# Optimization experiments

Hardware: AMD Instinct MI355X
Metric: run time of the kernel (lower is better)

The kernel has to match this reference:

```python
import jax, jax.numpy as jnp
import numpy as np

B, C_IN, C_OUT, T, R, CO = 8, 64, 64, 32, 32, 32


def setup_inputs() -> dict:
    key = jax.random.key(0)
    ks = jax.random.split(key, 8)
    scale = 1.0 / np.sqrt(C_IN)  # nn.Linear default uniform(-1/sqrt(in), 1/sqrt(in))
    w = lambda k: jax.random.uniform(k, (C_OUT, C_IN), jnp.float32, -scale, scale)
    return {
        "x": jax.random.normal(ks[0], (B, C_IN, T, R, CO), jnp.float32),
        "w_self": w(ks[1]),
        "w_tp": w(ks[2]),
        "w_tm": w(ks[3]),
        "w_rp": w(ks[4]),
        "w_rm": w(ks[5]),
        "w_cp": w(ks[6]),
        "w_cm": w(ks[7]),
    }


def _proj(v, w):
    # v: [B, t, r, c, C_in], w: [C_out, C_in] (nn.Linear layout)
    return jnp.einsum('btrci,oi->btrco', v, w)


def _shift_pad(a, axis, front):
    # pad 1 slice at front (True) or back (False) along `axis` of a 5-D tensor
    pads = [(0, 0)] * 5
    pads[axis] = (1, 0) if front else (0, 1)
    return jnp.pad(a, pads)


def reference(x, w_self, w_tp, w_tm, w_rp, w_rm, w_cp, w_cm):
    xp = jnp.transpose(x, (0, 2, 3, 4, 1))  # [B, T, R, Co, C_in]
    out = _proj(xp, w_self)
    if xp.shape[1] > 1:
        out = out + _shift_pad(_proj(xp[:, :-1], w_tp), 1, True)
        out = out + _shift_pad(_proj(xp[:, 1:], w_tm), 1, False)
    if xp.shape[2] > 1:
        out = out + _shift_pad(_proj(xp[:, :, :-1], w_rp), 2, True)
        out = out + _shift_pad(_proj(xp[:, :, 1:], w_rm), 2, False)
    if xp.shape[3] > 1:
        out = out + _shift_pad(_proj(xp[:, :, :, :-1], w_cp), 3, True)
        out = out + _shift_pad(_proj(xp[:, :, :, 1:], w_cm), 3, False)
    return jnp.transpose(out, (0, 4, 1, 2, 3))  # [B, C_out, T, R, Co]
```

## Files before the change

### kernel.cpp

```cpp
#include <hip/hip_runtime.h>


#define SB 32768
#define CIN 64
#define COUT 64
#define NB 8

typedef short s16x8 __attribute__((ext_vector_type(8)));
typedef __bf16 bf16x8 __attribute__((ext_vector_type(8)));
typedef float f32x4 __attribute__((ext_vector_type(4)));

__device__ __forceinline__ unsigned f2bf(float f) {
    unsigned u = __float_as_uint(f);
    u += 0x7FFFu + ((u >> 16) & 1u);
    return u >> 16;
}
__device__ __forceinline__ unsigned pk2(float lo, float hi) {
    return f2bf(lo) | (f2bf(hi) << 16);
}

__device__ __forceinline__ void gload_lds16(const void* g, void* l) {
    __builtin_amdgcn_global_load_lds(
        (const __attribute__((address_space(1))) void*)g,
        (__attribute__((address_space(3))) void*)l, 16, 0, 0);
}

__global__ __launch_bounds__(256) void prep2_kernel(const float* __restrict__ x,
                            const float* __restrict__ w0, const float* __restrict__ w1,
                            const float* __restrict__ w2, const float* __restrict__ w3,
                            const float* __restrict__ w4, const float* __restrict__ w5,
                            const float* __restrict__ w6,
                            unsigned short* __restrict__ ws) {
    int bid = blockIdx.x;
    int tid = threadIdx.x;
    if (bid >= 4096) {
        int tap = bid - 4096;
        const float* w = (tap == 0) ? w0 : (tap == 1) ? w1 : (tap == 2) ? w2
                       : (tap == 3) ? w3 : (tap == 4) ? w4 : (tap == 5) ? w5 : w6;
        unsigned p[8];
#pragma unroll
        for (int j = 0; j < 8; ++j)
            p[j] = pk2(w[tid * 16 + 2 * j], w[tid * 16 + 2 * j + 1]);
        uint4* dp = (uint4*)(ws + tap * 4096 + tid * 16);
        dp[0] = make_uint4(p[0], p[1], p[2], p[3]);
        dp[1] = make_uint4(p[4], p[5], p[6], p[7]);
        return;
    }
    int lbid = ((bid & 7) << 9) | (bid >> 3);
    int b = lbid >> 9;
    int i = (lbid & 511) * 256 + tid;
    int cg = i & 7;
    int s = (i >> 3) * 2;
    const float* xb = x + (size_t)b * CIN * SB;
    unsigned short* xq = ws + 7 * 4096;
    unsigned pa[4], pb[4];
#pragma unroll
    for (int u = 0; u < 4; ++u) {
        int ch = cg * 8 + 2 * u;
        float2 v0 = *(const float2*)(xb + (size_t)ch * SB + s);
        float2 v1 = *(const float2*)(xb + (size_t)(ch + 1) * SB + s);
        pa[u] = pk2(v0.x, v1.x);
        pb[u] = pk2(v0.y, v1.y);
    }
    uint4* dst = (uint4*)(xq + ((size_t)b * SB + s) * 64 + cg * 8);
    dst[0] = make_uint4(pa[0], pa[1], pa[2], pa[3]);
    dst[8] = make_uint4(pb[0], pb[1], pb[2], pb[3]);
}

__global__ __launch_bounds__(256, 2) void conv9_kernel(const unsigned short* __restrict__ xq,
                                                       const unsigned short* __restrict__ wq,
                                                       float* __restrict__ out) {
    __shared__ uint4 ring[4][640];
    int bid = blockIdx.x;
    int b = bid & 7;
    int rc0 = (bid >> 3) << 4;
    int tid = threadIdx.x;
    int lane = tid & 63;
    int wv = tid >> 6;
    int lo = lane & 15;
    int quad = lane >> 4;
    const uint4* xch = (const uint4*)(xq + (size_t)b * (CIN * SB));

    bf16x8 bq[7][2];
#pragma unroll
    for (int tap = 0; tap < 7; ++tap)
#pragma unroll
        for (int ks = 0; ks < 2; ++ks) {
            const unsigned short* bp = wq + tap * 4096
                + (wv * 16 + lo) * 64 + ks * 32 + quad * 8;
            bq[tap][ks] = __builtin_bit_cast(bf16x8, *(const s16x8*)bp);
        }

    int rc = rc0 + lo;
    int rl = 32 + lo;
    int r = (rc >> 5) & 31;
    int c = rc & 31;
    bool okrm = (r > 0), okrp = (r < 31), okcm = (c > 0), okcp = (c < 31);

    auto stage = [&](int ts, int k) {
#pragma unroll
        for (int j = 0; j < 2; ++j) {
            int cid = j * 256 + tid;
            int rw = cid >> 3;
            int sc = cid & 7;
            int rcx = rc0 - 32 + rw;
            rcx = rcx < 0 ? 0 : (rcx > 1023 ? 1023 : rcx);
            const uint4* g = xch + ((size_t)(ts * 1024 + rcx) << 3) + (sc ^ (rw & 7));
            gload_lds16((const void*)g, (void*)(&ring[k][j * 256 + (wv << 6)]));
        }
        if (wv < 2) {
            int cid = 512 + tid;
            int rw = cid >> 3;
            int sc = cid & 7;
            int rcx = rc0 - 32 + rw;
            rcx = rcx > 1023 ? 1023 : rcx;
            const uint4* g = xch + ((size_t)(ts * 1024 + rcx) << 3) + (sc ^ (rw & 7));
            gload_lds16((const void*)g, (void*)(&ring[k][512 + (wv << 6)]));
        }
    };

    const s16x8 zz = {0, 0, 0, 0, 0, 0, 0, 0};
    f32x4 acc;

    auto tap_lds = [&](const uint4* slab, const bf16x8 (&bt)[2], int d, bool ok) {
#pragma unroll
        for (int ks = 0; ks < 2; ++ks) {
            int row = rl + d;
            s16x8 a = *((const s16x8*)slab + row * 8 + ((ks * 4 + quad) ^ (row & 7)));
            a = ok ? a : zz;
            bf16x8 af = __builtin_bit_cast(bf16x8, a);
            acc = __builtin_amdgcn_mfma_f32_16x16x32_bf16(af, bt[ks], acc, 0, 0, 0);
        }
    };

    stage(0, 0);
    stage(1, 1);
    __syncthreads();

    for (int t = 0; t < 32; ++t) {
        if (t + 2 < 32) stage(t + 2, (t + 2) & 3);

        acc = (f32x4){0.f, 0.f, 0.f, 0.f};
        const uint4* sc_ = &ring[t & 3][0];

        tap_lds(sc_, bq[0], 0, true);
        if (t > 0)  tap_lds(&ring[(t - 1) & 3][0], bq[1], 0, true);
        if (t < 31) tap_lds(&ring[(t + 1) & 3][0], bq[2], 0, true);
        tap_lds(sc_, bq[3], -32, okrm);
        tap_lds(sc_, bq[4], 32, okrp);
        tap_lds(sc_, bq[5], -1, okcm);
        tap_lds(sc_, bq[6], 1, okcp);

        size_t ob = ((size_t)(b * COUT + wv * 16 + lo)) * SB
                  + (size_t)t * 1024 + rc0 + quad * 4;
        *(f32x4*)(out + ob) = acc;

        __syncthreads();
    }
}

__global__ __launch_bounds__(256) void wprep_kernel(const float* __restrict__ w0,
                            const float* __restrict__ w1, const float* __restrict__ w2,
                            const float* __restrict__ w3, const float* __restrict__ w4,
                            const float* __restrict__ w5, const float* __restrict__ w6,
                            unsigned short* __restrict__ ws) {
    int tap = blockIdx.x;
    int tid = threadIdx.x;
    const float* w = (tap == 0) ? w0 : (tap == 1) ? w1 : (tap == 2) ? w2
                   : (tap == 3) ? w3 : (tap == 4) ? w4 : (tap == 5) ? w5 : w6;
    unsigned p[8];
#pragma unroll
    for (int j = 0; j < 8; ++j)
        p[j] = pk2(w[tid * 16 + 2 * j], w[tid * 16 + 2 * j + 1]);
    uint4* dp = (uint4*)(ws + tap * 4096 + tid * 16);
    dp[0] = make_uint4(p[0], p[1], p[2], p[3]);
    dp[1] = make_uint4(p[4], p[5], p[6], p[7]);
}

__global__ __launch_bounds__(256) void conv_kernel(const float* __restrict__ x,
                                                   const unsigned short* __restrict__ wq,
                                                   float* __restrict__ out) {
    __shared__ uint4 alds[2560];
    int bid = blockIdx.x;
    int b = bid >> 7;
    int sblk = (bid & 127) << 8;
    int tid = threadIdx.x;
    const float* xb = x + (size_t)b * CIN * SB;

    {
        int rl = 32 + tid;
        const float* xp = xb + sblk + tid;
#pragma unroll
        for (int c = 0; c < 4; ++c) {
            unsigned pk[8];
#pragma unroll
            for (int u = 0; u < 8; ++u)
                pk[u] = pk2(xp[(size_t)(c * 16 + 2 * u) * SB],
                            xp[(size_t)(c * 16 + 2 * u + 1) * SB]);
            alds[rl * 8 + ((2 * c) ^ (rl & 7))] = make_uint4(pk[0], pk[1], pk[2], pk[3]);
            alds[rl * 8 + ((2 * c + 1) ^ (rl & 7))] = make_uint4(pk[4], pk[5], pk[6], pk[7]);
        }
    }
    {
        int hrow = tid & 63;
        int rl = (hrow < 32) ? hrow : hrow + 256;
        int s = sblk - 32 + rl;
        s = max(0, min(SB - 1, s));
        int ic = tid >> 6;
        const float* xp = xb + s + (size_t)(ic * 16) * SB;
        unsigned pk[8];
#pragma unroll
        for (int u = 0; u < 8; ++u)
            pk[u] = pk2(xp[(size_t)(2 * u) * SB], xp[(size_t)(2 * u + 1) * SB]);
        alds[rl * 8 + ((2 * ic) ^ (rl & 7))] = make_uint4(pk[0], pk[1], pk[2], pk[3]);
        alds[rl * 8 + ((2 * ic + 1) ^ (rl & 7))] = make_uint4(pk[4], pk[5], pk[6], pk[7]);
    }
    __syncthreads();

    int lane = tid & 63;
    int wv = tid >> 6;
    int lo = lane & 15;
    int quad = lane >> 4;
    int sbase = sblk + wv * 64;
    int t = sblk >> 10;

    f32x4 acc[4][4];
#pragma unroll
    for (int mt = 0; mt < 4; ++mt)
#pragma unroll
        for (int nt = 0; nt < 4; ++nt)
            acc[mt][nt] = (f32x4){0.f, 0.f, 0.f, 0.f};

    int r_m[4], c_m[4], rl[4];
#pragma unroll
    for (int mt = 0; mt < 4; ++mt) {
        int s = sbase + mt * 16 + lo;
        r_m[mt] = (s >> 5) & 31;
        c_m[mt] = s & 31;
        rl[mt] = s - sblk + 32;
    }

    auto load_b = [&](const unsigned short* wt, int ks, int nt) -> bf16x8 {
        const unsigned short* bp = wt + (nt * 16 + lo) * 64 + ks * 32 + quad * 8;
        return __builtin_bit_cast(bf16x8, *(const s16x8*)bp);
    };

    auto run_tap_lds = [&](int tap, int d, const bool ok[4]) {
        const unsigned short* wt = wq + tap * 4096;
#pragma unroll
        for (int ks = 0; ks < 2; ++ks) {
            bf16x8 bf[4];
#pragma unroll
            for (int nt = 0; nt < 4; ++nt) bf[nt] = load_b(wt, ks, nt);
            int j = ks * 4 + quad;
#pragma unroll
            for (int mt = 0; mt < 4; ++mt) {
                int row = rl[mt] + d;
                s16x8 raw = *((const s16x8*)alds + row * 8 + (j ^ (row & 7)));
                s16x8 zx = {0, 0, 0, 0, 0, 0, 0, 0};
                raw = ok[mt] ? raw : zx;
                bf16x8 af = __builtin_bit_cast(bf16x8, raw);
#pragma unroll
                for (int nt = 0; nt < 4; ++nt)
                    acc[mt][nt] = __builtin_amdgcn_mfma_f32_16x16x32_bf16(af, bf[nt], acc[mt][nt], 0, 0, 0);
            }
        }
    };

    auto run_tap_gather = [&](int tap, int d) {
        const unsigned short* wt = wq + tap * 4096;
#pragma unroll
        for (int ks = 0; ks < 2; ++ks) {
            bf16x8 bf[4];
#pragma unroll
            for (int nt = 0; nt < 4; ++nt) bf[nt] = load_b(wt, ks, nt);
            const float* gp = xb + (size_t)(ks * 32 + quad * 8) * SB + d;
#pragma unroll
            for (int mt = 0; mt < 4; ++mt) {
                const float* ap = gp + sbase + mt * 16 + lo;
                unsigned pk[4];
#pragma unroll
                for (int u = 0; u < 4; ++u)
                    pk[u] = pk2(ap[(size_t)(2 * u) * SB], ap[(size_t)(2 * u + 1) * SB]);
                uint4 v = make_uint4(pk[0], pk[1], pk[2], pk[3]);
                bf16x8 af = __builtin_bit_cast(bf16x8, v);
#pragma unroll
                for (int nt = 0; nt < 4; ++nt)
                    acc[mt][nt] = __builtin_amdgcn_mfma_f32_16x16x32_bf16(af, bf[nt], acc[mt][nt], 0, 0, 0);
            }
        }
    };

    {
        bool ok_all[4] = {true, true, true, true};
        run_tap_lds(0, 0, ok_all);
    }
    if (t > 0)  run_tap_gather(1, -1024);
    if (t < 31) run_tap_gather(2, 1024);
    {
        bool ok[4];
#pragma unroll
        for (int mt = 0; mt < 4; ++mt) ok[mt] = (r_m[mt] > 0);
        run_tap_lds(3, -32, ok);
#pragma unroll
        for (int mt = 0; mt < 4; ++mt) ok[mt] = (r_m[mt] < 31);
        run_tap_lds(4, 32, ok);
#pragma unroll
        for (int mt = 0; mt < 4; ++mt) ok[mt] = (c_m[mt] > 0);
        run_tap_lds(5, -1, ok);
#pragma unroll
        for (int mt = 0; mt < 4; ++mt) ok[mt] = (c_m[mt] < 31);
        run_tap_lds(6, 1, ok);
    }

#pragma unroll
    for (int mt = 0; mt < 4; ++mt) {
#pragma unroll
        for (int nt = 0; nt < 4; ++nt) {
            int o = nt * 16 + lo;
            size_t off = ((size_t)(b * COUT + o)) * SB + sbase + mt * 16 + quad * 4;
            *(f32x4*)(out + off) = acc[mt][nt];
        }
    }
}

__global__ void fallback_kernel(const float* __restrict__ x,
                                const float* __restrict__ w0, const float* __restrict__ w1,
                                const float* __restrict__ w2, const float* __restrict__ w3,
                                const float* __restrict__ w4, const float* __restrict__ w5,
                                const float* __restrict__ w6,
                                float* __restrict__ out) {
    int bid = blockIdx.x;
    int b = bid >> 11;
    int og = (bid >> 7) & 15;
    int sblk = (bid & 127) << 8;
    int tid = threadIdx.x;
    __shared__ float wl[7][4][64];
    const float* wp[7] = {w0, w1, w2, w3, w4, w5, w6};
    for (int k = tid; k < 7 * 4 * 64; k += 256) {
        int tap = k >> 8, oo = (k >> 6) & 3, i = k & 63;
        wl[tap][oo][i] = wp[tap][(og * 4 + oo) * 64 + i];
    }
    __syncthreads();
    int s = sblk + tid;
    int t = s >> 10, r = (s >> 5) & 31, c = s & 31;
    const float* xb = x + (size_t)b * CIN * SB + s;
    float a0 = 0, a1 = 0, a2 = 0, a3 = 0;
    for (int i = 0; i < 64; ++i) {
        const float* xi = xb + (size_t)i * SB;
        float vs = xi[0];
        float vtp = (t > 0) ? xi[-1024] : 0.f;
        float vtm = (t < 31) ? xi[1024] : 0.f;
        float vrp = (r > 0) ? xi[-32] : 0.f;
        float vrm = (r < 31) ? xi[32] : 0.f;
        float vcp = (c > 0) ? xi[-1] : 0.f;
        float vcm = (c < 31) ? xi[1] : 0.f;
        a0 += wl[0][0][i] * vs + wl[1][0][i] * vtp + wl[2][0][i] * vtm + wl[3][0][i] * vrp + wl[4][0][i] * vrm + wl[5][0][i] * vcp + wl[6][0][i] * vcm;
        a1 += wl[0][1][i] * vs + wl[1][1][i] * vtp + wl[2][1][i] * vtm + wl[3][1][i] * vrp + wl[4][1][i] * vrm + wl[5][1][i] * vcp + wl[6][1][i] * vcm;
        a2 += wl[0][2][i] * vs + wl[1][2][i] * vtp + wl[2][2][i] * vtm + wl[3][2][i] * vrp + wl[4][2][i] * vrm + wl[5][2][i] * vcp + wl[6][2][i] * vcm;
        a3 += wl[0][3][i] * vs + wl[1][3][i] * vtp + wl[2][3][i] * vtm + wl[3][3][i] * vrp + wl[4][3][i] * vrm + wl[5][3][i] * vcp + wl[6][3][i] * vcm;
    }
    size_t obase = ((size_t)b * COUT + og * 4) * SB + s;
    out[obase] = a0;
    out[obase + SB] = a1;
    out[obase + 2 * (size_t)SB] = a2;
    out[obase + 3 * (size_t)SB] = a3;
}

extern "C" void kernel_launch(void* const* d_in, const int* in_sizes, int n_in,
                              void* d_out, int out_size, void* d_ws, size_t ws_size,
                              hipStream_t stream) {
    const float* x = (const float*)d_in[0];
    const float* w0 = (const float*)d_in[1];
    const float* w1 = (const float*)d_in[2];
    const float* w2 = (const float*)d_in[3];
    const float* w3 = (const float*)d_in[4];
    const float* w4 = (const float*)d_in[5];
    const float* w5 = (const float*)d_in[6];
    const float* w6 = (const float*)d_in[7];
    float* out = (float*)d_out;

    size_t need_w = (size_t)7 * 4096 * 2;
    size_t need_full = need_w + (size_t)NB * CIN * SB * 2;
    if (d_ws != nullptr && ws_size >= need_full) {
        unsigned short* wsp = (unsigned short*)d_ws;
        prep2_kernel<<<4103, 256, 0, stream>>>(x, w0, w1, w2, w3, w4, w5, w6, wsp);
        conv9_kernel<<<512, 256, 0, stream>>>(wsp + 7 * 4096, wsp, out);
    } else if (d_ws != nullptr && ws_size >= need_w) {
        unsigned short* wsp = (unsigned short*)d_ws;
        wprep_kernel<<<7, 256, 0, stream>>>(w0, w1, w2, w3, w4, w5, w6, wsp);
        conv_kernel<<<1024, 256, 0, stream>>>(x, wsp, out);
    } else {
        fallback_kernel<<<8 * 16 * 128, 256, 0, stream>>>(x, w0, w1, w2, w3, w4, w5, w6, out);
    }
}
```

Measured before the change: 158.0 us.

## Double conv block tile to 32 positions with 512 threads and split accumulators

Each block now covers 32 spatial positions instead of 16 and runs 512 threads across 256 blocks. The x slab staged per time step grows only from 80 to 96 rows, so there is less halo overfetch per output. Each tap's two K-halves now feed two independent MFMA accumulators that are summed at the store, which shortens the dependent MFMA chain. The trailing __syncthreads is replaced by an explicit vmcnt wait plus barrier at the top of each iteration. That wait may be conservative because stores share the counter, and it halves the number of blocks available for occupancy.

```diff
diff --git a/kernel.cpp b/kernel.cpp
--- a/kernel.cpp
+++ b/kernel.cpp
@@ -67,18 +67,20 @@
     dst[8] = make_uint4(pb[0], pb[1], pb[2], pb[3]);
 }
 
-__global__ __launch_bounds__(256, 2) void conv9_kernel(const unsigned short* __restrict__ xq,
-                                                       const unsigned short* __restrict__ wq,
-                                                       float* __restrict__ out) {
-    __shared__ uint4 ring[4][640];
+__global__ __launch_bounds__(512, 2) void conv10_kernel(const unsigned short* __restrict__ xq,
+                                                        const unsigned short* __restrict__ wq,
+                                                        float* __restrict__ out) {
+    __shared__ uint4 ring[4][768];
     int bid = blockIdx.x;
     int b = bid & 7;
-    int rc0 = (bid >> 3) << 4;
+    int rc0 = (bid >> 3) << 5;
     int tid = threadIdx.x;
     int lane = tid & 63;
     int wv = tid >> 6;
     int lo = lane & 15;
     int quad = lane >> 4;
+    int oq = wv & 3;
+    int rh = wv >> 2;
     const uint4* xch = (const uint4*)(xq + (size_t)b * (CIN * SB));
 
     bf16x8 bq[7][2];
@@ -87,28 +89,27 @@
 #pragma unroll
         for (int ks = 0; ks < 2; ++ks) {
             const unsigned short* bp = wq + tap * 4096
-                + (wv * 16 + lo) * 64 + ks * 32 + quad * 8;
+                + (oq * 16 + lo) * 64 + ks * 32 + quad * 8;
             bq[tap][ks] = __builtin_bit_cast(bf16x8, *(const s16x8*)bp);
         }
 
-    int rc = rc0 + lo;
-    int rl = 32 + lo;
+    int rc = rc0 + rh * 16 + lo;
+    int rl = 32 + rh * 16 + lo;
     int r = (rc >> 5) & 31;
     int c = rc & 31;
     bool okrm = (r > 0), okrp = (r < 31), okcm = (c > 0), okcp = (c < 31);
 
     auto stage = [&](int ts, int k) {
-#pragma unroll
-        for (int j = 0; j < 2; ++j) {
-            int cid = j * 256 + tid;
+        {
+            int cid = tid;
             int rw = cid >> 3;
             int sc = cid & 7;
             int rcx = rc0 - 32 + rw;
             rcx = rcx < 0 ? 0 : (rcx > 1023 ? 1023 : rcx);
             const uint4* g = xch + ((size_t)(ts * 1024 + rcx) << 3) + (sc ^ (rw & 7));
-            gload_lds16((const void*)g, (void*)(&ring[k][j * 256 + (wv << 6)]));
-        }
-        if (wv < 2) {
+            gload_lds16((const void*)g, (void*)(&ring[k][wv << 6]));
+        }
+        if (wv < 4) {
             int cid = 512 + tid;
             int rw = cid >> 3;
             int sc = cid & 7;
@@ -120,27 +121,32 @@
     };
 
     const s16x8 zz = {0, 0, 0, 0, 0, 0, 0, 0};
-    f32x4 acc;
+    f32x4 acc_a, acc_b;
 
     auto tap_lds = [&](const uint4* slab, const bf16x8 (&bt)[2], int d, bool ok) {
-#pragma unroll
-        for (int ks = 0; ks < 2; ++ks) {
-            int row = rl + d;
-            s16x8 a = *((const s16x8*)slab + row * 8 + ((ks * 4 + quad) ^ (row & 7)));
-            a = ok ? a : zz;
-            bf16x8 af = __builtin_bit_cast(bf16x8, a);
-            acc = __builtin_amdgcn_mfma_f32_16x16x32_bf16(af, bt[ks], acc, 0, 0, 0);
-        }
+        int row = rl + d;
+        s16x8 a0 = *((const s16x8*)slab + row * 8 + ((quad) ^ (row & 7)));
+        s16x8 a1 = *((const s16x8*)slab + row * 8 + ((4 + quad) ^ (row & 7)));
+        a0 = ok ? a0 : zz;
+        a1 = ok ? a1 : zz;
+        acc_a = __builtin_amdgcn_mfma_f32_16x16x32_bf16(__builtin_bit_cast(bf16x8, a0), bt[0], acc_a, 0, 0, 0);
+        acc_b = __builtin_amdgcn_mfma_f32_16x16x32_bf16(__builtin_bit_cast(bf16x8, a1), bt[1], acc_b, 0, 0, 0);
     };
 
     stage(0, 0);
     stage(1, 1);
-    __syncthreads();
+    asm volatile("s_waitcnt vmcnt(0)" ::: "memory");
+    __builtin_amdgcn_s_barrier();
 
     for (int t = 0; t < 32; ++t) {
+        asm volatile("s_waitcnt vmcnt(1)" ::: "memory");
+        __builtin_amdgcn_s_barrier();
+        __builtin_amdgcn_sched_barrier(0);
+
         if (t + 2 < 32) stage(t + 2, (t + 2) & 3);
 
-        acc = (f32x4){0.f, 0.f, 0.f, 0.f};
+        acc_a = (f32x4){0.f, 0.f, 0.f, 0.f};
+        acc_b = (f32x4){0.f, 0.f, 0.f, 0.f};
         const uint4* sc_ = &ring[t & 3][0];
 
         tap_lds(sc_, bq[0], 0, true);
@@ -151,11 +157,9 @@
         tap_lds(sc_, bq[5], -1, okcm);
         tap_lds(sc_, bq[6], 1, okcp);
 
-        size_t ob = ((size_t)(b * COUT + wv * 16 + lo)) * SB
-                  + (size_t)t * 1024 + rc0 + quad * 4;
-        *(f32x4*)(out + ob) = acc;
-
-        __syncthreads();
+        size_t ob = ((size_t)(b * COUT + oq * 16 + lo)) * SB
+                  + (size_t)t * 1024 + rc0 + rh * 16 + quad * 4;
+        *(f32x4*)(out + ob) = acc_a + acc_b;
     }
 }
 
@@ -385,7 +389,7 @@
     if (d_ws != nullptr && ws_size >= need_full) {
         unsigned short* wsp = (unsigned short*)d_ws;
         prep2_kernel<<<4103, 256, 0, stream>>>(x, w0, w1, w2, w3, w4, w5, w6, wsp);
-        conv9_kernel<<<512, 256, 0, stream>>>(wsp + 7 * 4096, wsp, out);
+        conv10_kernel<<<256, 512, 0, stream>>>(wsp + 7 * 4096, wsp, out);
     } else if (d_ws != nullptr && ws_size >= need_w) {
         unsigned short* wsp = (unsigned short*)d_ws;
         wprep_kernel<<<7, 256, 0, stream>>>(w0, w1, w2, w3, w4, w5, w6, wsp);
```

After: 151.5 us. -4.1%, faster.
